# Performance work log

Hardware: AMD Instinct MI355X
Metric: run time of the kernel (lower is better)

Reference implementation:

```python
import jax, jax.numpy as jnp
import numpy as np

DEN_LEAKY = 1e-05
NUM_LEAKY = 1e-20


def _chain_objf(xexp, lengths, e_in, e_out, e_pdf, e_prob, leaky, final, coeff):
    """Leaky-HMM forward recursion (pychain forward_backward objective).

    xexp: [B,T,D] exp'd clamped network outputs
    e_*:  edge lists, either shared [E] or per-utterance [B,E]
    leaky/final: [S] or [B,S]
    Returns scalar objf = sum_b log p(X_b | graph_b).
    """
    B, T, D = xexp.shape
    if leaky.ndim == 1:
        leaky = jnp.broadcast_to(leaky[None, :], (B, leaky.shape[0]))
        final = jnp.broadcast_to(final[None, :], (B, final.shape[0]))
    S = leaky.shape[1]
    if e_in.ndim == 1:
        E = e_in.shape[0]
        e_in = jnp.broadcast_to(e_in[None, :], (B, E))
        e_out = jnp.broadcast_to(e_out[None, :], (B, E))
        e_pdf = jnp.broadcast_to(e_pdf[None, :], (B, E))
        e_prob = jnp.broadcast_to(e_prob[None, :], (B, E))
    seg = (e_out + S * jnp.arange(B, dtype=e_out.dtype)[:, None]).ravel()

    # alpha at t=0: mass 1 on start_state (0), plus leaky mass (alpha_sum = 1)
    alpha0 = jnp.zeros((B, S), xexp.dtype).at[:, 0].set(1.0)
    alpha0 = alpha0 + coeff * leaky

    mask_t = jnp.arange(T)[:, None] < lengths[None, :]  # [T,B] ragged frame mask

    def step(carry, inp):
        alpha, logz = carry
        xt, m = inp  # xt: [B,D], m: [B]
        # transition scores: alpha[src] * graph_prob * exp_logit[pdf]
        vals = (jnp.take_along_axis(alpha, e_in, axis=1)
                * e_prob
                * jnp.take_along_axis(xt, e_pdf, axis=1))  # [B,E]
        anew = jax.ops.segment_sum(vals.ravel(), seg, num_segments=B * S).reshape(B, S)
        asum = anew.sum(-1, keepdims=True)  # [B,1] per-frame arbitrary scale
        adash = (anew + coeff * leaky * asum) / asum  # leaky-HMM + renorm
        alpha = jnp.where(m[:, None], adash, alpha)
        logz = logz + jnp.where(m, jnp.log(asum[:, 0]), 0.0)
        return (alpha, logz), None

    (alpha, logz), _ = jax.lax.scan(
        step, (alpha0, jnp.zeros((B,), xexp.dtype)),
        (jnp.transpose(xexp, (1, 0, 2)), mask_t))
    return jnp.sum(logz + jnp.log(jnp.sum(alpha * final, axis=-1)))


def setup_inputs() -> dict:
    key = jax.random.key(0)
    ks = jax.random.split(key, 12)
    B, T, D = 32, 400, 2048
    S_den, E_den = 2000, 60000
    S_num, E_num = 512, 2048
    x = jax.random.normal(ks[0], (B, T, D), dtype=jnp.float32)
    x_lengths = jnp.clip(T - jnp.arange(B, dtype=jnp.int32) * 8, 32, T)  # sorted desc
    den_e_in = jax.random.randint(ks[1], (E_den,), 0, S_den, dtype=jnp.int32)
    den_e_out = jax.random.randint(ks[2], (E_den,), 0, S_den, dtype=jnp.int32)
    den_e_pdf = jax.random.randint(ks[3], (E_den,), 0, D, dtype=jnp.int32)
    den_e_prob = jax.random.uniform(ks[4], (E_den,), dtype=jnp.float32, minval=0.05, maxval=1.0)
    den_leaky = jax.random.uniform(ks[5], (S_den,), dtype=jnp.float32, minval=0.01, maxval=1.0)
    den_final = jax.random.uniform(ks[6], (S_den,), dtype=jnp.float32, minval=0.1, maxval=1.0)
    num_e_in = jax.random.randint(ks[7], (B, E_num), 0, S_num, dtype=jnp.int32)
    num_e_out = jax.random.randint(ks[8], (B, E_num), 0, S_num, dtype=jnp.int32)
    num_e_pdf = jax.random.randint(ks[9], (B, E_num), 0, D, dtype=jnp.int32)
    num_e_prob = jax.random.uniform(ks[10], (B, E_num), dtype=jnp.float32, minval=0.05, maxval=1.0)
    k11, k12 = jax.random.split(ks[11])
    num_leaky = jax.random.uniform(k11, (B, S_num), dtype=jnp.float32, minval=0.01, maxval=1.0)
    num_final = jax.random.uniform(k12, (B, S_num), dtype=jnp.float32, minval=0.1, maxval=1.0)
    return {"x": x, "x_lengths": x_lengths,
            "den_e_in": den_e_in, "den_e_out": den_e_out, "den_e_pdf": den_e_pdf,
            "den_e_prob": den_e_prob, "den_leaky": den_leaky, "den_final": den_final,
            "num_e_in": num_e_in, "num_e_out": num_e_out, "num_e_pdf": num_e_pdf,
            "num_e_prob": num_e_prob, "num_leaky": num_leaky, "num_final": num_final}


def reference(x, x_lengths, den_e_in, den_e_out, den_e_pdf, den_e_prob, den_leaky,
              den_final, num_e_in, num_e_out, num_e_pdf, num_e_prob, num_leaky,
              num_final):
    xexp = jnp.exp(jnp.clip(x, -30.0, 30.0))
    den_objf = _chain_objf(xexp, x_lengths, den_e_in, den_e_out, den_e_pdf,
                           den_e_prob, den_leaky, den_final, DEN_LEAKY)
    num_objf = _chain_objf(xexp, x_lengths, num_e_in, num_e_out, num_e_pdf,
                           num_e_prob, num_leaky, num_final, NUM_LEAKY)
    objf = -(num_objf - den_objf)
    return objf / x_lengths.sum().astype(x.dtype)
```

## Files before the change

### kernel.cpp

```cpp
#include <hip/hip_runtime.h>
#include <math.h>

#define B_SZ   32
#define T_SZ   400
#define D_SZ   2048
#define S_DEN  2000
#define E_DEN  60000
#define S_NUM  512
#define E_NUM  2048
#define DEN_C  1e-5f
#define NUM_C  1e-20f

#define P_CH   4
#define NTHR   512
#define EPT    32
#define EPC    16384

#define REC_OFF     0u
#define ANEWG_OFF   0u
#define PACK_OFF    960000u
#define ROWPTR_OFF  1484288u
#define CNT_OFF     1492352u
#define SROW_OFF    1492352u
#define CUR_OFF     1500352u
#define RSPLIT_OFF  1508352u
#define PSUM_OFF    1508416u
#define CTR_OFF     1510464u
#define TOTD_OFF    1512512u
#define TOTN_OFF    1512640u
#define WS_BYTES    1512768u

__device__ __forceinline__ float expclip(float v) {
    return __expf(fminf(fmaxf(v, -30.f), 30.f));
}
__device__ __forceinline__ float ldf_agent(const float* p) {
    return __hip_atomic_load(p, __ATOMIC_RELAXED, __HIP_MEMORY_SCOPE_AGENT);
}
__device__ __forceinline__ int ldi_agent(const int* p) {
    return __hip_atomic_load(p, __ATOMIC_RELAXED, __HIP_MEMORY_SCOPE_AGENT);
}
__device__ __forceinline__ void stf_agent(float* p, float v) {
    __hip_atomic_store(p, v, __ATOMIC_RELAXED, __HIP_MEMORY_SCOPE_AGENT);
}

__global__ void prep_init(char* ws) {
    int tid = threadIdx.x;
    int* cnt = (int*)(ws + CNT_OFF);
    int* cur = (int*)(ws + CUR_OFF);
    for (int i = tid; i < S_DEN; i += 256) { cnt[i] = 0; cur[i] = 0; }
    if (tid < B_SZ) ((int*)(ws + CTR_OFF))[tid << 4] = 0;
}

__global__ void prep_hist(const int* __restrict__ e_out, char* ws) {
    int e = blockIdx.x * blockDim.x + threadIdx.x;
    if (e < E_DEN) atomicAdd((int*)(ws + CNT_OFF) + e_out[e], 1);
}

__global__ __launch_bounds__(1024) void prep_scan(char* ws) {
    __shared__ int sb[2][2048];
    const int* cnt = (const int*)(ws + CNT_OFF);
    int* rowp = (int*)(ws + ROWPTR_OFF);
    int tid = threadIdx.x;
    for (int i = tid; i < 2048; i += 1024) sb[0][i] = (i < S_DEN) ? cnt[i] : 0;
    __syncthreads();
    int cur = 0;
    for (int d = 1; d < 2048; d <<= 1) {
        for (int i = tid; i < 2048; i += 1024)
            sb[1 - cur][i] = sb[cur][i] + ((i >= d) ? sb[cur][i - d] : 0);
        __syncthreads();
        cur ^= 1;
    }
    if (tid == 0) rowp[0] = 0;
    for (int i = tid; i < S_DEN; i += 1024) rowp[i + 1] = sb[cur][i];
    __syncthreads();
    if (tid == 0) {
        int* rs = (int*)(ws + RSPLIT_OFF);
        rs[0] = 0; rs[P_CH] = S_DEN;
        for (int p = 1; p < P_CH; ++p) {
            int target = (E_DEN / P_CH) * p;
            int lo = 0, hi = S_DEN;
            while (lo < hi) {
                int mid = (lo + hi) >> 1;
                int v = (mid == 0) ? 0 : sb[cur][mid - 1];
                if (v >= target) hi = mid; else lo = mid + 1;
            }
            rs[p] = lo;
        }
    }
}

__global__ void prep_scatter(const int* __restrict__ e_in, const int* __restrict__ e_out,
                             const int* __restrict__ e_pdf, const float* __restrict__ e_prob,
                             char* ws) {
    int e = blockIdx.x * blockDim.x + threadIdx.x;
    if (e >= E_DEN) return;
    const int* rowp = (const int*)(ws + ROWPTR_OFF);
    int* cur = (int*)(ws + CUR_OFF);
    int4* recs = (int4*)(ws + REC_OFF);
    int o = e_out[e];
    int pos = rowp[o] + atomicAdd(&cur[o], 1);
    int4 r;
    r.x = e_in[e]; r.y = e_pdf[e];
    r.z = __float_as_int(e_prob[e]);
    r.w = o;
    recs[pos] = r;
}

__global__ void prep_pack(char* ws) {
    int slot = blockIdx.x * blockDim.x + threadIdx.x;
    if (slot >= P_CH * EPC) return;
    int p = slot >> 14;
    int k = slot & (EPC - 1);
    const int* rowp = (const int*)(ws + ROWPTR_OFF);
    const int* rs = (const int*)(ws + RSPLIT_OFF);
    int ebase = rowp[rs[p]], eend = rowp[rs[p + 1]];
    uint2* pk = (uint2*)(ws + PACK_OFF);
    int idx = ebase + k;
    uint2 val;
    int myrow;
    if (idx < eend) {
        const int4* r4 = (const int4*)(ws + REC_OFF);
        int4 r = r4[idx];
        myrow = r.w;
        int nxt = (idx + 1 < eend) ? r4[idx + 1].w : myrow;
        unsigned d = (unsigned)(nxt - myrow);
        if (d > 1023u) d = 1023u;
        val = make_uint2((unsigned)r.x | ((unsigned)r.y << 11) | (d << 22),
                         (unsigned)r.z);
    } else {
        val = make_uint2(0u, 0u);
        myrow = rs[p];
    }
    pk[slot] = val;
    if ((k & (EPT - 1)) == 0)
        ((int*)(ws + SROW_OFF))[(p << 9) + (k >> 5)] = myrow;
}

__global__ __launch_bounds__(NTHR, 2) void chain_fwd5(
    const float* __restrict__ x, const int* __restrict__ lengths,
    const float* __restrict__ den_leaky, const float* __restrict__ den_final,
    const int* __restrict__ num_in, const int* __restrict__ num_out,
    const int* __restrict__ num_pdf, const float* __restrict__ num_prob,
    const float* __restrict__ num_leaky, const float* __restrict__ num_final,
    char* __restrict__ ws)
{
    __shared__ float alpha[2048];
    __shared__ float xrow[2048];
    __shared__ float anew[2048];
    __shared__ float red[16];
    extern __shared__ float dynpad[];
    const int tid = threadIdx.x;
    if (lengths[0] == -12345) dynpad[tid] = 1.f;

    if (blockIdx.x < P_CH * B_SZ) {
        const int b = blockIdx.x & (B_SZ - 1);
        const int p = blockIdx.x >> 5;
        const int len = lengths[b];
        const float* xb = x + (size_t)b * T_SZ * D_SZ;
        const int* rs = (const int*)(ws + RSPLIT_OFF);
        const int rlo = rs[p], rhi = rs[p + 1];
        float* anewg = (float*)(ws + ANEWG_OFF) + ((size_t)(b << 1) << 11);
        float* psumg = (float*)(ws + PSUM_OFF);
        int* ctr = (int*)(ws + CTR_OFF) + (b << 4);

        float lc[4], fc[4];
        #pragma unroll
        for (int i = 0; i < 4; ++i) {
            int s = tid + (i << 9);
            lc[i] = (s < S_DEN) ? DEN_C * den_leaky[s] : 0.f;
            fc[i] = (s < S_DEN) ? den_final[s] : 0.f;
        }
        #pragma unroll
        for (int i = 0; i < 4; ++i) {
            int s = tid + (i << 9);
            alpha[s] = lc[i] + ((s == 0) ? 1.f : 0.f);
            anew[s] = 0.f;
            xrow[s] = expclip(xb[s]);
        }

        const uint4* __restrict__ pk4 = (const uint4*)(ws + PACK_OFF);
        const int qb = (p << 13) + (tid << 4);
        const int row0 = ((const int*)(ws + SROW_OFF))[(p << 9) + tid];
        float logz = 0.f;
        uint4 c0 = pk4[qb + 0], c1 = pk4[qb + 1], c2 = pk4[qb + 2], c3 = pk4[qb + 3];
        uint4 c4 = pk4[qb + 4], c5 = pk4[qb + 5], c6 = pk4[qb + 6], c7 = pk4[qb + 7];
        __syncthreads();

        for (int t = 0; t < len; ++t) {
            const int par = t & 1;
            const int tn = (t + 1 < len) ? t + 1 : t;
            const float* xq = xb + (size_t)tn * D_SZ;
            const float xn0 = xq[tid], xn1 = xq[tid + 512];
            const float xn2 = xq[tid + 1024], xn3 = xq[tid + 1536];

            float acc = 0.f, psum = 0.f;
            int row = row0;
            #pragma unroll
            for (int sb = 0; sb < 2; ++sb) {
                const int nq = qb + (((sb + 1) & 1) << 3);
                uint4 n0 = pk4[nq + 0], n1 = pk4[nq + 1], n2 = pk4[nq + 2], n3 = pk4[nq + 3];
                uint4 n4 = pk4[nq + 4], n5 = pk4[nq + 5], n6 = pk4[nq + 6], n7 = pk4[nq + 7];
                const unsigned w[16] = {c0.x, c0.z, c1.x, c1.z, c2.x, c2.z, c3.x, c3.z,
                                        c4.x, c4.z, c5.x, c5.z, c6.x, c6.z, c7.x, c7.z};
                const unsigned pr[16] = {c0.y, c0.w, c1.y, c1.w, c2.y, c2.w, c3.y, c3.w,
                                         c4.y, c4.w, c5.y, c5.w, c6.y, c6.w, c7.y, c7.w};
                float av[16], xv[16];
                #pragma unroll
                for (int i = 0; i < 16; ++i) av[i] = alpha[w[i] & 2047u];
                #pragma unroll
                for (int i = 0; i < 16; ++i) xv[i] = xrow[(w[i] >> 11) & 2047u];
                #pragma unroll
                for (int i = 0; i < 16; ++i) {
                    acc = __fmaf_rn(av[i] * __uint_as_float(pr[i]), xv[i], acc);
                    const unsigned d = w[i] >> 22;
                    if (d) { psum += acc; atomicAdd(&anew[row], acc); acc = 0.f; row += (int)d; }
                }
                c0 = n0; c1 = n1; c2 = n2; c3 = n3;
                c4 = n4; c5 = n5; c6 = n6; c7 = n7;
            }
            psum += acc;
            if (acc != 0.f) atomicAdd(&anew[row], acc);

            #pragma unroll
            for (int o = 32; o > 0; o >>= 1) psum += __shfl_down(psum, o, 64);
            if ((tid & 63) == 0) red[tid >> 6] = psum;
            __syncthreads();

            float* ag = anewg + (par << 11);
            const int pidx = (b << 4) | (par << 3);
            if (tid == 0) {
                float bs = red[0]+red[1]+red[2]+red[3]+red[4]+red[5]+red[6]+red[7];
                stf_agent(&psumg[pidx + p], bs);
            }
            for (int r = rlo + tid; r < rhi; r += NTHR) {
                stf_agent(&ag[r], anew[r]); anew[r] = 0.f;
            }
            asm volatile("s_waitcnt vmcnt(0)" ::: "memory");
            if ((tid & 63) == 0)
                __hip_atomic_fetch_add(ctr, 1, __ATOMIC_RELAXED, __HIP_MEMORY_SCOPE_AGENT);

            xrow[tid]        = expclip(xn0);
            xrow[tid + 512]  = expclip(xn1);
            xrow[tid + 1024] = expclip(xn2);
            xrow[tid + 1536] = expclip(xn3);

            if (tid < 64) {
                const int target = (P_CH * (NTHR / 64)) * (t + 1);
                int gd = 0;
                while (ldi_agent(ctr) < target) {
                    __builtin_amdgcn_s_sleep(1);
                    if (++gd > (1 << 15)) break;
                }
                if (tid < 4) red[8 + tid] = ldf_agent(&psumg[pidx + tid]);
            }
            __syncthreads();

            const float asum = red[8] + red[9] + red[10] + red[11];
            const float inv = 1.f / asum;
            #pragma unroll
            for (int i = 0; i < 4; ++i) {
                const int s = tid + (i << 9);
                float an = (s < S_DEN) ? ldf_agent(&ag[s]) : 0.f;
                alpha[s] = __fmaf_rn(an, inv, lc[i]);
            }
            logz += logf(asum);
            __syncthreads();
        }

        if (p == 0) {
            float fs = alpha[tid] * fc[0] + alpha[tid + 512] * fc[1]
                     + alpha[tid + 1024] * fc[2] + alpha[tid + 1536] * fc[3];
            #pragma unroll
            for (int o = 32; o > 0; o >>= 1) fs += __shfl_down(fs, o, 64);
            if ((tid & 63) == 0) red[tid >> 6] = fs;
            __syncthreads();
            if (tid == 0) {
                float tot = red[0]+red[1]+red[2]+red[3]+red[4]+red[5]+red[6]+red[7];
                ((float*)(ws + TOTD_OFF))[b] = logz + logf(tot);
            }
        }
    } else {
        const int b = blockIdx.x - P_CH * B_SZ;
        const int len = lengths[b];
        const float* xb = x + (size_t)b * T_SZ * D_SZ;
        float* nalpha = alpha;
        float* nanew  = anew;
        const float lk = num_leaky[(b << 9) + tid];
        const float fn = num_final[(b << 9) + tid];
        int ein[4], eout[4], epdf[4]; float eprb[4];
        #pragma unroll
        for (int k = 0; k < 4; ++k) {
            int e = (b << 11) + tid + (k << 9);
            ein[k] = num_in[e]; eout[k] = num_out[e];
            epdf[k] = num_pdf[e]; eprb[k] = num_prob[e];
        }
        nalpha[tid] = NUM_C * lk + ((tid == 0) ? 1.f : 0.f);
        nanew[tid] = 0.f;
        #pragma unroll
        for (int i = 0; i < 4; ++i) xrow[tid + (i << 9)] = expclip(xb[tid + (i << 9)]);
        float logz = 0.f;
        __syncthreads();

        for (int t = 0; t < len; ++t) {
            const int tn = (t + 1 < len) ? t + 1 : t;
            const float* xq = xb + (size_t)tn * D_SZ;
            const float xn0 = xq[tid], xn1 = xq[tid + 512];
            const float xn2 = xq[tid + 1024], xn3 = xq[tid + 1536];
            #pragma unroll
            for (int k = 0; k < 4; ++k) {
                float v = nalpha[ein[k]] * eprb[k] * xrow[epdf[k]];
                atomicAdd(&nanew[eout[k]], v);
            }
            __syncthreads();
            float ps = nanew[tid];
            #pragma unroll
            for (int o = 32; o > 0; o >>= 1) ps += __shfl_down(ps, o, 64);
            if ((tid & 63) == 0) red[tid >> 6] = ps;
            __syncthreads();
            float asum = 0.f;
            #pragma unroll
            for (int i = 0; i < 8; ++i) asum += red[i];
            nalpha[tid] = __fmaf_rn(NUM_C * lk, asum, nanew[tid]) * (1.f / asum);
            nanew[tid] = 0.f;
            xrow[tid]        = expclip(xn0);
            xrow[tid + 512]  = expclip(xn1);
            xrow[tid + 1024] = expclip(xn2);
            xrow[tid + 1536] = expclip(xn3);
            logz += logf(asum);
            __syncthreads();
        }
        float fs = nalpha[tid] * fn;
        #pragma unroll
        for (int o = 32; o > 0; o >>= 1) fs += __shfl_down(fs, o, 64);
        if ((tid & 63) == 0) red[tid >> 6] = fs;
        __syncthreads();
        if (tid == 0) {
            float tot = 0.f;
            #pragma unroll
            for (int i = 0; i < 8; ++i) tot += red[i];
            ((float*)(ws + TOTN_OFF))[b] = logz + logf(tot);
        }
    }
}

__global__ void combine2(const char* __restrict__ ws, const int* __restrict__ lengths,
                         float* __restrict__ out) {
    const float* totd = (const float*)(ws + TOTD_OFF);
    const float* totn = (const float*)(ws + TOTN_OFF);
    int tid = threadIdx.x;
    float v = 0.f, l = 0.f;
    if (tid < B_SZ) { v = totd[tid] - totn[tid]; l = (float)lengths[tid]; }
    #pragma unroll
    for (int o = 32; o > 0; o >>= 1) { v += __shfl_down(v, o, 64); l += __shfl_down(l, o, 64); }
    if (tid == 0) out[0] = v / l;
}

__global__ __launch_bounds__(1024) void chain_fwd_kernel(
    const float* __restrict__ x, const int* __restrict__ lengths,
    const int* __restrict__ den_in, const int* __restrict__ den_out,
    const int* __restrict__ den_pdf, const float* __restrict__ den_prob,
    const float* __restrict__ den_leaky, const float* __restrict__ den_final,
    const int* __restrict__ num_in, const int* __restrict__ num_out,
    const int* __restrict__ num_pdf, const float* __restrict__ num_prob,
    const float* __restrict__ num_leaky, const float* __restrict__ num_final,
    float* __restrict__ part)
{
    __shared__ float xrow[D_SZ];
    __shared__ float alpha[S_DEN];
    __shared__ float anew[S_DEN];
    __shared__ float red[17];
    const int tid = threadIdx.x;
    const int nthr = 1024;
    const bool is_den = blockIdx.x < B_SZ;
    const int b = blockIdx.x & (B_SZ - 1);
    int S, E;
    const int *e_in, *e_out, *e_pdf;
    const float *e_prob, *leaky, *fin;
    float coeff;
    if (is_den) {
        S = S_DEN; E = E_DEN;
        e_in = den_in; e_out = den_out; e_pdf = den_pdf; e_prob = den_prob;
        leaky = den_leaky; fin = den_final; coeff = DEN_C;
    } else {
        S = S_NUM; E = E_NUM;
        e_in = num_in + b * E_NUM; e_out = num_out + b * E_NUM;
        e_pdf = num_pdf + b * E_NUM; e_prob = num_prob + b * E_NUM;
        leaky = num_leaky + b * S_NUM; fin = num_final + b * S_NUM;
        coeff = NUM_C;
    }
    const int len = lengths[b];
    const float* xb = x + (size_t)b * T_SZ * D_SZ;
    for (int s = tid; s < S; s += nthr)
        alpha[s] = coeff * leaky[s] + (s == 0 ? 1.0f : 0.0f);
    float logz = 0.0f;
    for (int t = 0; t < len; ++t) {
        for (int s = tid; s < S; s += nthr) anew[s] = 0.0f;
        const float* xt = xb + (size_t)t * D_SZ;
        for (int d = tid; d < D_SZ; d += nthr)
            xrow[d] = __expf(fminf(fmaxf(xt[d], -30.0f), 30.0f));
        __syncthreads();
        for (int e = tid; e < E; e += nthr) {
            float v = alpha[e_in[e]] * e_prob[e] * xrow[e_pdf[e]];
            atomicAdd(&anew[e_out[e]], v);
        }
        __syncthreads();
        float ps = 0.0f;
        for (int s = tid; s < S; s += nthr) ps += anew[s];
        #pragma unroll
        for (int off = 32; off > 0; off >>= 1) ps += __shfl_down(ps, off, 64);
        if ((tid & 63) == 0) red[tid >> 6] = ps;
        __syncthreads();
        if (tid < 64) {
            float v = (tid < 16) ? red[tid] : 0.0f;
            #pragma unroll
            for (int off = 8; off > 0; off >>= 1) v += __shfl_down(v, off, 64);
            if (tid == 0) red[16] = v;
        }
        __syncthreads();
        const float asum = red[16];
        const float inv = 1.0f / asum;
        for (int s = tid; s < S; s += nthr)
            alpha[s] = (anew[s] + coeff * leaky[s] * asum) * inv;
        logz += logf(asum);
        __syncthreads();
    }
    float fs = 0.0f;
    for (int s = tid; s < S; s += nthr) fs += alpha[s] * fin[s];
    #pragma unroll
    for (int off = 32; off > 0; off >>= 1) fs += __shfl_down(fs, off, 64);
    if ((tid & 63) == 0) red[tid >> 6] = fs;
    __syncthreads();
    if (tid < 64) {
        float v = (tid < 16) ? red[tid] : 0.0f;
        #pragma unroll
        for (int off = 8; off > 0; off >>= 1) v += __shfl_down(v, off, 64);
        if (tid == 0) part[blockIdx.x] = logz + logf(v);
    }
}

__global__ void combine_kernel(const float* __restrict__ part,
                               const int* __restrict__ lengths,
                               float* __restrict__ out)
{
    int tid = threadIdx.x;
    float v = 0.0f, l = 0.0f;
    if (tid < B_SZ) { v = part[tid] - part[B_SZ + tid]; l = (float)lengths[tid]; }
    #pragma unroll
    for (int off = 32; off > 0; off >>= 1) { v += __shfl_down(v, off, 64); l += __shfl_down(l, off, 64); }
    if (tid == 0) out[0] = v / l;
}

extern "C" void kernel_launch(void* const* d_in, const int* in_sizes, int n_in,
                              void* d_out, int out_size, void* d_ws, size_t ws_size,
                              hipStream_t stream)
{
    const float* x          = (const float*)d_in[0];
    const int*   lengths    = (const int*)  d_in[1];
    const int*   den_in_p   = (const int*)  d_in[2];
    const int*   den_out_p  = (const int*)  d_in[3];
    const int*   den_pdf_p  = (const int*)  d_in[4];
    const float* den_prob_p = (const float*)d_in[5];
    const float* den_leaky  = (const float*)d_in[6];
    const float* den_final  = (const float*)d_in[7];
    const int*   num_in_p   = (const int*)  d_in[8];
    const int*   num_out_p  = (const int*)  d_in[9];
    const int*   num_pdf_p  = (const int*)  d_in[10];
    const float* num_prob_p = (const float*)d_in[11];
    const float* num_leaky  = (const float*)d_in[12];
    const float* num_final  = (const float*)d_in[13];

    if (ws_size >= WS_BYTES) {
        char* ws = (char*)d_ws;
        hipLaunchKernelGGL(prep_init, dim3(1), dim3(256), 0, stream, ws);
        hipLaunchKernelGGL(prep_hist, dim3((E_DEN + 255) / 256), dim3(256), 0, stream,
                           den_out_p, ws);
        hipLaunchKernelGGL(prep_scan, dim3(1), dim3(1024), 0, stream, ws);
        hipLaunchKernelGGL(prep_scatter, dim3((E_DEN + 255) / 256), dim3(256), 0, stream,
                           den_in_p, den_out_p, den_pdf_p, den_prob_p, ws);
        hipLaunchKernelGGL(prep_pack, dim3((P_CH * EPC + 255) / 256), dim3(256), 0, stream, ws);
        hipLaunchKernelGGL(chain_fwd5, dim3(P_CH * B_SZ + B_SZ), dim3(NTHR), 60000, stream,
                           x, lengths, den_leaky, den_final,
                           num_in_p, num_out_p, num_pdf_p, num_prob_p,
                           num_leaky, num_final, ws);
        hipLaunchKernelGGL(combine2, dim3(1), dim3(64), 0, stream,
                           ws, lengths, (float*)d_out);
    } else {
        float* part = (float*)d_ws;
        hipLaunchKernelGGL(chain_fwd_kernel, dim3(2 * B_SZ), dim3(1024), 0, stream,
                           x, lengths,
                           den_in_p, den_out_p, den_pdf_p, den_prob_p, den_leaky, den_final,
                           num_in_p, num_out_p, num_pdf_p, num_prob_p, num_leaky, num_final,
                           part);
        hipLaunchKernelGGL(combine_kernel, dim3(1), dim3(64), 0, stream,
                           part, lengths, (float*)d_out);
    }
}
```

Before: 2.792 ms.

## Split denominator graph across eight blocks per utterance and fold numerator into one

```diff
diff --git a/kernel.cpp b/kernel.cpp
--- a/kernel.cpp
+++ b/kernel.cpp
@@ -11,24 +11,25 @@
 #define DEN_C  1e-5f
 #define NUM_C  1e-20f
 
-#define P_CH   4
+#define P_CH   8
 #define NTHR   512
-#define EPT    32
-#define EPC    16384
+#define EPT    16
+#define EPC    8192
 
 #define REC_OFF     0u
 #define ANEWG_OFF   0u
 #define PACK_OFF    960000u
 #define ROWPTR_OFF  1484288u
 #define CNT_OFF     1492352u
-#define SROW_OFF    1492352u
 #define CUR_OFF     1500352u
-#define RSPLIT_OFF  1508352u
-#define PSUM_OFF    1508416u
-#define CTR_OFF     1510464u
-#define TOTD_OFF    1512512u
-#define TOTN_OFF    1512640u
-#define WS_BYTES    1512768u
+#define SROW_OFF    1508352u
+#define RSPLIT_OFF  1524736u
+#define PSUM_OFF    1524800u
+#define CTR_OFF     1528896u
+#define XCD_OFF     1530944u
+#define TOTD_OFF    1531968u
+#define TOTN_OFF    1532096u
+#define WS_BYTES    1532224u
 
 __device__ __forceinline__ float expclip(float v) {
     return __expf(fminf(fmaxf(v, -30.f), 30.f));
@@ -40,6 +41,9 @@
     return __hip_atomic_load(p, __ATOMIC_RELAXED, __HIP_MEMORY_SCOPE_AGENT);
 }
 __device__ __forceinline__ void stf_agent(float* p, float v) {
+    __hip_atomic_store(p, v, __ATOMIC_RELAXED, __HIP_MEMORY_SCOPE_AGENT);
+}
+__device__ __forceinline__ void sti_agent(int* p, int v) {
     __hip_atomic_store(p, v, __ATOMIC_RELAXED, __HIP_MEMORY_SCOPE_AGENT);
 }
 
@@ -48,7 +52,10 @@
     int* cnt = (int*)(ws + CNT_OFF);
     int* cur = (int*)(ws + CUR_OFF);
     for (int i = tid; i < S_DEN; i += 256) { cnt[i] = 0; cur[i] = 0; }
-    if (tid < B_SZ) ((int*)(ws + CTR_OFF))[tid << 4] = 0;
+    int* ctr = (int*)(ws + CTR_OFF);
+    for (int i = tid; i < B_SZ * 16; i += 256) ctr[i] = 0;
+    int* xcd = (int*)(ws + XCD_OFF);
+    if (tid < B_SZ * 8) xcd[tid] = 0;
 }
 
 __global__ void prep_hist(const int* __restrict__ e_out, char* ws) {
@@ -109,7 +116,7 @@
 __global__ void prep_pack(char* ws) {
     int slot = blockIdx.x * blockDim.x + threadIdx.x;
     if (slot >= P_CH * EPC) return;
-    int p = slot >> 14;
+    int p = slot >> 13;
     int k = slot & (EPC - 1);
     const int* rowp = (const int*)(ws + ROWPTR_OFF);
     const int* rs = (const int*)(ws + RSPLIT_OFF);
@@ -133,10 +140,10 @@
     }
     pk[slot] = val;
     if ((k & (EPT - 1)) == 0)
-        ((int*)(ws + SROW_OFF))[(p << 9) + (k >> 5)] = myrow;
-}
-
-__global__ __launch_bounds__(NTHR, 2) void chain_fwd5(
+        ((int*)(ws + SROW_OFF))[(p << 9) + (k >> 4)] = myrow;
+}
+
+__global__ __launch_bounds__(NTHR, 2) void chain_fwd6(
     const float* __restrict__ x, const int* __restrict__ lengths,
     const float* __restrict__ den_leaky, const float* __restrict__ den_final,
     const int* __restrict__ num_in, const int* __restrict__ num_out,
@@ -147,198 +154,203 @@
     __shared__ float alpha[2048];
     __shared__ float xrow[2048];
     __shared__ float anew[2048];
-    __shared__ float red[16];
+    __shared__ float nalpha[S_NUM];
+    __shared__ float nanew[S_NUM];
+    __shared__ float red[24];
+    __shared__ int sSame;
     extern __shared__ float dynpad[];
     const int tid = threadIdx.x;
     if (lengths[0] == -12345) dynpad[tid] = 1.f;
 
-    if (blockIdx.x < P_CH * B_SZ) {
-        const int b = blockIdx.x & (B_SZ - 1);
-        const int p = blockIdx.x >> 5;
-        const int len = lengths[b];
-        const float* xb = x + (size_t)b * T_SZ * D_SZ;
-        const int* rs = (const int*)(ws + RSPLIT_OFF);
-        const int rlo = rs[p], rhi = rs[p + 1];
-        float* anewg = (float*)(ws + ANEWG_OFF) + ((size_t)(b << 1) << 11);
-        float* psumg = (float*)(ws + PSUM_OFF);
-        int* ctr = (int*)(ws + CTR_OFF) + (b << 4);
-
-        float lc[4], fc[4];
-        #pragma unroll
-        for (int i = 0; i < 4; ++i) {
-            int s = tid + (i << 9);
-            lc[i] = (s < S_DEN) ? DEN_C * den_leaky[s] : 0.f;
-            fc[i] = (s < S_DEN) ? den_final[s] : 0.f;
-        }
-        #pragma unroll
-        for (int i = 0; i < 4; ++i) {
-            int s = tid + (i << 9);
-            alpha[s] = lc[i] + ((s == 0) ? 1.f : 0.f);
-            anew[s] = 0.f;
-            xrow[s] = expclip(xb[s]);
-        }
-
-        const uint4* __restrict__ pk4 = (const uint4*)(ws + PACK_OFF);
-        const int qb = (p << 13) + (tid << 4);
-        const int row0 = ((const int*)(ws + SROW_OFF))[(p << 9) + tid];
-        float logz = 0.f;
-        uint4 c0 = pk4[qb + 0], c1 = pk4[qb + 1], c2 = pk4[qb + 2], c3 = pk4[qb + 3];
-        uint4 c4 = pk4[qb + 4], c5 = pk4[qb + 5], c6 = pk4[qb + 6], c7 = pk4[qb + 7];
-        __syncthreads();
-
-        for (int t = 0; t < len; ++t) {
-            const int par = t & 1;
-            const int tn = (t + 1 < len) ? t + 1 : t;
-            const float* xq = xb + (size_t)tn * D_SZ;
-            const float xn0 = xq[tid], xn1 = xq[tid + 512];
-            const float xn2 = xq[tid + 1024], xn3 = xq[tid + 1536];
-
-            float acc = 0.f, psum = 0.f;
-            int row = row0;
-            #pragma unroll
-            for (int sb = 0; sb < 2; ++sb) {
-                const int nq = qb + (((sb + 1) & 1) << 3);
-                uint4 n0 = pk4[nq + 0], n1 = pk4[nq + 1], n2 = pk4[nq + 2], n3 = pk4[nq + 3];
-                uint4 n4 = pk4[nq + 4], n5 = pk4[nq + 5], n6 = pk4[nq + 6], n7 = pk4[nq + 7];
-                const unsigned w[16] = {c0.x, c0.z, c1.x, c1.z, c2.x, c2.z, c3.x, c3.z,
-                                        c4.x, c4.z, c5.x, c5.z, c6.x, c6.z, c7.x, c7.z};
-                const unsigned pr[16] = {c0.y, c0.w, c1.y, c1.w, c2.y, c2.w, c3.y, c3.w,
-                                         c4.y, c4.w, c5.y, c5.w, c6.y, c6.w, c7.y, c7.w};
-                float av[16], xv[16];
-                #pragma unroll
-                for (int i = 0; i < 16; ++i) av[i] = alpha[w[i] & 2047u];
-                #pragma unroll
-                for (int i = 0; i < 16; ++i) xv[i] = xrow[(w[i] >> 11) & 2047u];
-                #pragma unroll
-                for (int i = 0; i < 16; ++i) {
-                    acc = __fmaf_rn(av[i] * __uint_as_float(pr[i]), xv[i], acc);
-                    const unsigned d = w[i] >> 22;
-                    if (d) { psum += acc; atomicAdd(&anew[row], acc); acc = 0.f; row += (int)d; }
-                }
-                c0 = n0; c1 = n1; c2 = n2; c3 = n3;
-                c4 = n4; c5 = n5; c6 = n6; c7 = n7;
-            }
-            psum += acc;
-            if (acc != 0.f) atomicAdd(&anew[row], acc);
-
-            #pragma unroll
-            for (int o = 32; o > 0; o >>= 1) psum += __shfl_down(psum, o, 64);
-            if ((tid & 63) == 0) red[tid >> 6] = psum;
-            __syncthreads();
-
-            float* ag = anewg + (par << 11);
-            const int pidx = (b << 4) | (par << 3);
-            if (tid == 0) {
-                float bs = red[0]+red[1]+red[2]+red[3]+red[4]+red[5]+red[6]+red[7];
-                stf_agent(&psumg[pidx + p], bs);
-            }
-            for (int r = rlo + tid; r < rhi; r += NTHR) {
-                stf_agent(&ag[r], anew[r]); anew[r] = 0.f;
-            }
-            asm volatile("s_waitcnt vmcnt(0)" ::: "memory");
-            if ((tid & 63) == 0)
-                __hip_atomic_fetch_add(ctr, 1, __ATOMIC_RELAXED, __HIP_MEMORY_SCOPE_AGENT);
-
-            xrow[tid]        = expclip(xn0);
-            xrow[tid + 512]  = expclip(xn1);
-            xrow[tid + 1024] = expclip(xn2);
-            xrow[tid + 1536] = expclip(xn3);
-
-            if (tid < 64) {
-                const int target = (P_CH * (NTHR / 64)) * (t + 1);
-                int gd = 0;
-                while (ldi_agent(ctr) < target) {
-                    __builtin_amdgcn_s_sleep(1);
-                    if (++gd > (1 << 15)) break;
-                }
-                if (tid < 4) red[8 + tid] = ldf_agent(&psumg[pidx + tid]);
-            }
-            __syncthreads();
-
-            const float asum = red[8] + red[9] + red[10] + red[11];
-            const float inv = 1.f / asum;
-            #pragma unroll
-            for (int i = 0; i < 4; ++i) {
-                const int s = tid + (i << 9);
-                float an = (s < S_DEN) ? ldf_agent(&ag[s]) : 0.f;
-                alpha[s] = __fmaf_rn(an, inv, lc[i]);
-            }
-            logz += logf(asum);
-            __syncthreads();
-        }
-
-        if (p == 0) {
-            float fs = alpha[tid] * fc[0] + alpha[tid + 512] * fc[1]
-                     + alpha[tid + 1024] * fc[2] + alpha[tid + 1536] * fc[3];
-            #pragma unroll
-            for (int o = 32; o > 0; o >>= 1) fs += __shfl_down(fs, o, 64);
-            if ((tid & 63) == 0) red[tid >> 6] = fs;
-            __syncthreads();
-            if (tid == 0) {
-                float tot = red[0]+red[1]+red[2]+red[3]+red[4]+red[5]+red[6]+red[7];
-                ((float*)(ws + TOTD_OFF))[b] = logz + logf(tot);
-            }
-        }
-    } else {
-        const int b = blockIdx.x - P_CH * B_SZ;
-        const int len = lengths[b];
-        const float* xb = x + (size_t)b * T_SZ * D_SZ;
-        float* nalpha = alpha;
-        float* nanew  = anew;
-        const float lk = num_leaky[(b << 9) + tid];
-        const float fn = num_final[(b << 9) + tid];
-        int ein[4], eout[4], epdf[4]; float eprb[4];
+    const int b = blockIdx.x & (B_SZ - 1);
+    const int p = blockIdx.x >> 5;
+    const bool isNum = (p == 0);
+    const int len = lengths[b];
+    const float* xb = x + (size_t)b * T_SZ * D_SZ;
+    const int* rs = (const int*)(ws + RSPLIT_OFF);
+    const int rlo = rs[p], rhi = rs[p + 1];
+    float* anewg = (float*)(ws + ANEWG_OFF) + ((size_t)(b << 1) << 11);
+    float* psumg = (float*)(ws + PSUM_OFF);
+    int* ctr = (int*)(ws + CTR_OFF) + (b << 4);
+    int* xcdArr = (int*)(ws + XCD_OFF);
+
+    int myxcc = 0;
+    asm volatile("s_getreg_b32 %0, hwreg(HW_REG_XCC_ID)" : "=s"(myxcc));
+    if (tid == 0) {
+        sti_agent(&xcdArr[(b << 3) + p], myxcc + 1);
+        asm volatile("s_waitcnt vmcnt(0)" ::: "memory");
+        __hip_atomic_fetch_add(ctr + 1, 1, __ATOMIC_RELAXED, __HIP_MEMORY_SCOPE_AGENT);
+    }
+    if (tid < 64) {
+        int gd = 0;
+        while (ldi_agent(ctr + 1) < P_CH) {
+            __builtin_amdgcn_s_sleep(2);
+            if (++gd > (1 << 16)) break;
+        }
+        int v = (tid < 8) ? ldi_agent(&xcdArr[(b << 3) + tid]) : -1;
+        int v0 = __shfl(v, 0, 64);
+        bool eq = (tid < 8) ? (v == v0 && v != 0) : true;
+        unsigned long long m = __ballot(eq);
+        if (tid == 0) sSame = (~m == 0ULL) ? 1 : 0;
+    }
+
+    float lc[4], fc[4];
+    #pragma unroll
+    for (int i = 0; i < 4; ++i) {
+        int s = tid + (i << 9);
+        lc[i] = (s < S_DEN) ? DEN_C * den_leaky[s] : 0.f;
+        fc[i] = (s < S_DEN) ? den_final[s] : 0.f;
+    }
+    #pragma unroll
+    for (int i = 0; i < 4; ++i) {
+        int s = tid + (i << 9);
+        alpha[s] = lc[i] + ((s == 0) ? 1.f : 0.f);
+        anew[s] = 0.f;
+        xrow[s] = expclip(xb[s]);
+    }
+
+    float nlk = 0.f, nfn = 0.f, nlogz = 0.f;
+    int nein[4], neout[4], nepdf[4]; float neprb[4];
+    if (isNum) {
+        nlk = num_leaky[(b << 9) + tid];
+        nfn = num_final[(b << 9) + tid];
         #pragma unroll
         for (int k = 0; k < 4; ++k) {
             int e = (b << 11) + tid + (k << 9);
-            ein[k] = num_in[e]; eout[k] = num_out[e];
-            epdf[k] = num_pdf[e]; eprb[k] = num_prob[e];
-        }
-        nalpha[tid] = NUM_C * lk + ((tid == 0) ? 1.f : 0.f);
+            nein[k] = num_in[e]; neout[k] = num_out[e];
+            nepdf[k] = num_pdf[e]; neprb[k] = num_prob[e];
+        }
+        nalpha[tid] = NUM_C * nlk + ((tid == 0) ? 1.f : 0.f);
         nanew[tid] = 0.f;
-        #pragma unroll
-        for (int i = 0; i < 4; ++i) xrow[tid + (i << 9)] = expclip(xb[tid + (i << 9)]);
-        float logz = 0.f;
-        __syncthreads();
-
-        for (int t = 0; t < len; ++t) {
-            const int tn = (t + 1 < len) ? t + 1 : t;
-            const float* xq = xb + (size_t)tn * D_SZ;
-            const float xn0 = xq[tid], xn1 = xq[tid + 512];
-            const float xn2 = xq[tid + 1024], xn3 = xq[tid + 1536];
+    }
+
+    const uint4* __restrict__ pk4 = (const uint4*)(ws + PACK_OFF);
+    const int qb = (p << 12) + (tid << 3);
+    const uint4 c0 = pk4[qb + 0], c1 = pk4[qb + 1], c2 = pk4[qb + 2], c3 = pk4[qb + 3];
+    const uint4 c4 = pk4[qb + 4], c5 = pk4[qb + 5], c6 = pk4[qb + 6], c7 = pk4[qb + 7];
+    const int row0 = ((const int*)(ws + SROW_OFF))[(p << 9) + tid];
+    float logz = 0.f;
+    __syncthreads();
+    const bool fastSt = (sSame != 0);
+
+    for (int t = 0; t < len; ++t) {
+        const int par = t & 1;
+        const int tn = (t + 1 < len) ? t + 1 : t;
+        const float* xq = xb + (size_t)tn * D_SZ;
+        const float xn0 = xq[tid], xn1 = xq[tid + 512];
+        const float xn2 = xq[tid + 1024], xn3 = xq[tid + 1536];
+
+        float acc = 0.f, psum = 0.f;
+        int row = row0;
+        {
+            const unsigned w[16] = {c0.x, c0.z, c1.x, c1.z, c2.x, c2.z, c3.x, c3.z,
+                                    c4.x, c4.z, c5.x, c5.z, c6.x, c6.z, c7.x, c7.z};
+            const unsigned pr[16] = {c0.y, c0.w, c1.y, c1.w, c2.y, c2.w, c3.y, c3.w,
+                                     c4.y, c4.w, c5.y, c5.w, c6.y, c6.w, c7.y, c7.w};
+            float av[16], xv[16];
+            #pragma unroll
+            for (int i = 0; i < 16; ++i) av[i] = alpha[w[i] & 2047u];
+            #pragma unroll
+            for (int i = 0; i < 16; ++i) xv[i] = xrow[(w[i] >> 11) & 2047u];
+            #pragma unroll
+            for (int i = 0; i < 16; ++i) {
+                acc = __fmaf_rn(av[i] * __uint_as_float(pr[i]), xv[i], acc);
+                const unsigned d = w[i] >> 22;
+                if (d) { psum += acc; atomicAdd(&anew[row], acc); acc = 0.f; row += (int)d; }
+            }
+        }
+        psum += acc;
+        if (acc != 0.f) atomicAdd(&anew[row], acc);
+        #pragma unroll
+        for (int o = 32; o > 0; o >>= 1) psum += __shfl_down(psum, o, 64);
+        if ((tid & 63) == 0) red[tid >> 6] = psum;
+        __syncthreads();
+
+        float* ag = anewg + (par << 11);
+        const int pidx = ((b << 1) | par) << 4;
+        if (tid == 0) {
+            float bs = red[0]+red[1]+red[2]+red[3]+red[4]+red[5]+red[6]+red[7];
+            if (fastSt) psumg[pidx + p] = bs;
+            else        stf_agent(&psumg[pidx + p], bs);
+        }
+        if (fastSt) {
+            for (int r = rlo + tid; r < rhi; r += NTHR) { ag[r] = anew[r]; anew[r] = 0.f; }
+        } else {
+            for (int r = rlo + tid; r < rhi; r += NTHR) { stf_agent(&ag[r], anew[r]); anew[r] = 0.f; }
+        }
+        asm volatile("s_waitcnt vmcnt(0)" ::: "memory");
+        if ((tid & 63) == 0)
+            __hip_atomic_fetch_add(ctr, 1, __ATOMIC_RELAXED, __HIP_MEMORY_SCOPE_AGENT);
+
+        if (isNum) {
             #pragma unroll
             for (int k = 0; k < 4; ++k) {
-                float v = nalpha[ein[k]] * eprb[k] * xrow[epdf[k]];
-                atomicAdd(&nanew[eout[k]], v);
+                float v = nalpha[nein[k]] * neprb[k] * xrow[nepdf[k]];
+                atomicAdd(&nanew[neout[k]], v);
             }
             __syncthreads();
             float ps = nanew[tid];
             #pragma unroll
             for (int o = 32; o > 0; o >>= 1) ps += __shfl_down(ps, o, 64);
-            if ((tid & 63) == 0) red[tid >> 6] = ps;
-            __syncthreads();
-            float asum = 0.f;
-            #pragma unroll
-            for (int i = 0; i < 8; ++i) asum += red[i];
-            nalpha[tid] = __fmaf_rn(NUM_C * lk, asum, nanew[tid]) * (1.f / asum);
+            if ((tid & 63) == 0) red[8 + (tid >> 6)] = ps;
+        }
+
+        xrow[tid]        = expclip(xn0);
+        xrow[tid + 512]  = expclip(xn1);
+        xrow[tid + 1024] = expclip(xn2);
+        xrow[tid + 1536] = expclip(xn3);
+
+        if (tid < 64) {
+            const int target = (P_CH * (NTHR / 64)) * (t + 1);
+            int gd = 0;
+            while (ldi_agent(ctr) < target) {
+                __builtin_amdgcn_s_sleep(1);
+                if (++gd > (1 << 15)) break;
+            }
+            if (tid < 8) red[16 + tid] = ldf_agent(&psumg[pidx + tid]);
+        }
+        __syncthreads();
+
+        const float asum = red[16]+red[17]+red[18]+red[19]
+                         + red[20]+red[21]+red[22]+red[23];
+        const float inv = 1.f / asum;
+        #pragma unroll
+        for (int i = 0; i < 4; ++i) {
+            const int s = tid + (i << 9);
+            float an = (s < S_DEN) ? ldf_agent(&ag[s]) : 0.f;
+            alpha[s] = __fmaf_rn(an, inv, lc[i]);
+        }
+        logz += logf(asum);
+        if (isNum) {
+            const float nasum = red[8]+red[9]+red[10]+red[11]
+                              + red[12]+red[13]+red[14]+red[15];
+            nalpha[tid] = __fmaf_rn(NUM_C * nlk, nasum, nanew[tid]) * (1.f / nasum);
             nanew[tid] = 0.f;
-            xrow[tid]        = expclip(xn0);
-            xrow[tid + 512]  = expclip(xn1);
-            xrow[tid + 1024] = expclip(xn2);
-            xrow[tid + 1536] = expclip(xn3);
-            logz += logf(asum);
-            __syncthreads();
-        }
-        float fs = nalpha[tid] * fn;
+            nlogz += logf(nasum);
+        }
+        __syncthreads();
+    }
+
+    if (isNum) {
+        float fs = alpha[tid] * fc[0] + alpha[tid + 512] * fc[1]
+                 + alpha[tid + 1024] * fc[2] + alpha[tid + 1536] * fc[3];
         #pragma unroll
         for (int o = 32; o > 0; o >>= 1) fs += __shfl_down(fs, o, 64);
         if ((tid & 63) == 0) red[tid >> 6] = fs;
         __syncthreads();
         if (tid == 0) {
-            float tot = 0.f;
-            #pragma unroll
-            for (int i = 0; i < 8; ++i) tot += red[i];
-            ((float*)(ws + TOTN_OFF))[b] = logz + logf(tot);
+            float tot = red[0]+red[1]+red[2]+red[3]+red[4]+red[5]+red[6]+red[7];
+            ((float*)(ws + TOTD_OFF))[b] = logz + logf(tot);
+        }
+        __syncthreads();
+        float nfs = nalpha[tid] * nfn;
+        #pragma unroll
+        for (int o = 32; o > 0; o >>= 1) nfs += __shfl_down(nfs, o, 64);
+        if ((tid & 63) == 0) red[tid >> 6] = nfs;
+        __syncthreads();
+        if (tid == 0) {
+            float tot = red[0]+red[1]+red[2]+red[3]+red[4]+red[5]+red[6]+red[7];
+            ((float*)(ws + TOTN_OFF))[b] = nlogz + logf(tot);
         }
     }
 }
@@ -478,7 +490,7 @@
         hipLaunchKernelGGL(prep_scatter, dim3((E_DEN + 255) / 256), dim3(256), 0, stream,
                            den_in_p, den_out_p, den_pdf_p, den_prob_p, ws);
         hipLaunchKernelGGL(prep_pack, dim3((P_CH * EPC + 255) / 256), dim3(256), 0, stream, ws);
-        hipLaunchKernelGGL(chain_fwd5, dim3(P_CH * B_SZ + B_SZ), dim3(NTHR), 60000, stream,
+        hipLaunchKernelGGL(chain_fwd6, dim3(P_CH * B_SZ), dim3(NTHR), 57344, stream,
                            x, lengths, den_leaky, den_final,
                            num_in_p, num_out_p, num_pdf_p, num_prob_p,
                            num_leaky, num_final, ws);
```

Measured after the change: 2.710 ms. 2.9% less time.
